# Kernel tuning notes

Hardware: AMD Instinct MI355X
Metric: run time of the kernel (lower is better)

## Reference

```python
import jax, jax.numpy as jnp
import numpy as np
import math

S, D, H, L, V = 1024, 768, 12, 6, 32000
KD = D // H
FF = 4 * D
PAD = 0


def setup_inputs() -> dict:
    key = jax.random.key(0)
    ks = jax.random.split(key, 20)
    s = D ** -0.5
    return {
        "token_ids": jax.random.randint(ks[0], (2, S), 0, V, dtype=jnp.int32),
        "emb": jax.random.normal(ks[1], (V, D)) * s,
        "Wq": jax.random.normal(ks[2], (L, H, D, KD)) * s,
        "bq": jnp.zeros((L, H, KD)),
        "Wk": jax.random.normal(ks[3], (L, H, D, KD)) * s,
        "bk": jnp.zeros((L, H, KD)),
        "Wv": jax.random.normal(ks[4], (L, H, D, D)) * s,
        "bv": jnp.zeros((L, H, D)),
        "g1": jnp.ones((L, D)), "be1": jnp.zeros((L, D)),
        "g2": jnp.ones((L, D)), "be2": jnp.zeros((L, D)),
        "W1": jax.random.normal(ks[5], (L, D, FF)) * s,
        "b1": jnp.zeros((L, FF)),
        "W2": jax.random.normal(ks[6], (L, FF, D)) * (FF ** -0.5),
        "b2": jnp.zeros((L, D)),
        "Wout": jax.random.normal(ks[7], (D, V)) * s,
        "bout": jnp.zeros((V,)),
    }


def _pe():
    pos = jnp.arange(S, dtype=jnp.float32)[:, None]
    div = jnp.exp(jnp.arange(0, D, 2, dtype=jnp.float32) * (-math.log(10000.0) / D))
    ang = pos * div  # [S, D/2]
    return jnp.stack([jnp.sin(ang), jnp.cos(ang)], axis=-1).reshape(S, D)


def _ln(x, g, b):
    m = x.mean(-1, keepdims=True)
    v = ((x - m) ** 2).mean(-1, keepdims=True)
    return (x - m) * jax.lax.rsqrt(v + 1e-5) * g + b


def reference(token_ids, emb, Wq, bq, Wk, bk, Wv, bv, g1, be1, g2, be2, W1, b1, W2, b2, Wout, bout):
    pad = token_ids == PAD  # [B,S]
    causal = jnp.triu(jnp.ones((S, S), dtype=bool), k=1)
    # mask[b,s,t] = causal | pad-as-key | pad-as-query
    mask = causal[None, None] | pad[:, None, None, :] | pad[:, None, :, None]  # [B,1,S,S]
    scale = math.sqrt(KD)
    x = emb[token_ids] + _pe()[None]  # [B,S,D]
    for l in range(L):
        q = jnp.einsum('bsd,hdk->bhsk', x, Wq[l]) + bq[l][None, :, None, :]
        k = jnp.einsum('bsd,hdk->bhsk', x, Wk[l]) + bk[l][None, :, None, :]
        v = jnp.einsum('bsd,hde->bhse', x, Wv[l]) + bv[l][None, :, None, :]
        scores = jnp.einsum('bhsk,bhtk->bhst', q, k) / scale
        scores = jnp.where(mask, -jnp.inf, scores)
        all_masked = jnp.all(mask, axis=-1)  # rows with every key masked -> uniform attn
        scores = jnp.where(all_masked[..., None], 0.0, scores)
        attn = jax.nn.softmax(scores, axis=-1)
        heads = jnp.einsum('bhst,bhte->bhse', attn, v)  # per-head full-D values
        attn_out = heads.mean(axis=1)  # heads are AVERAGED, not concatenated
        x = _ln(x + attn_out, g1[l], be1[l])
        ff = jax.nn.relu(x @ W1[l] + b1[l]) @ W2[l] + b2[l]
        x = _ln(x + ff, g2[l], be2[l])
    return x @ Wout + bout
```

## Files before the change

### kernel.cpp

```cpp
#include <hip/hip_runtime.h>
#include <hip/hip_bf16.h>

#define SQ 1024
#define DM 768
#define NH 12
#define NL 6
#define NV 32000
#define KDH 64
#define FFD 3072

using bf16 = __hip_bfloat16;
typedef __attribute__((ext_vector_type(4))) float f32x4;
typedef __attribute__((ext_vector_type(8))) short bf16x8;

__global__ void fill_kernel(float* __restrict__ out, long n, float val) {
  const long stride = (long)gridDim.x * blockDim.x;
  for (long i = (long)blockIdx.x * blockDim.x + threadIdx.x; i < n; i += stride)
    out[i] = val;
}

__device__ __forceinline__ void gload16(const void* g, void* l) {
  __builtin_amdgcn_global_load_lds(
      (const __attribute__((address_space(1))) unsigned int*)g,
      (__attribute__((address_space(3))) unsigned int*)l, 16, 0, 0);
}

template<bool OUT_BF16, bool RELU, bool CSKIP = false, bool CTRUNC = false>
__global__ __launch_bounds__(256) void gemm_bt(
    int M, int N, int K,
    const bf16* __restrict__ Ap, long sAz, int lda,
    const bf16* __restrict__ Bp, long sBz, int ldbt,
    const float* __restrict__ biasp, int sBiasZ,
    void* __restrict__ Cp, long sCz, long sCb, long sCs, long sCn)
{
  __shared__ __align__(16) char lds[49152];

  const int tid = threadIdx.x;
  const int gx = gridDim.x, gy = gridDim.y;
  const int nwg = gx * gy * (int)gridDim.z;
  int flat = ((int)blockIdx.z * gy + (int)blockIdx.y) * gx + (int)blockIdx.x;
  {
    const int q = nwg >> 3, r = nwg & 7;
    const int xcd = flat & 7, loc = flat >> 3;
    flat = (xcd < r ? xcd * (q + 1) : r * (q + 1) + (xcd - r) * q) + loc;
  }
  const int bx  = flat % gx;
  const int byz = flat / gx;
  const int m0 = bx * 128;
  const int n0 = (byz % gy) * 128;
  const int z  = byz / gy;

  if (CSKIP && n0 > m0) return;
  const int KK = CTRUNC ? min(K, m0 + 128) : K;

  const int lane = tid & 63;
  const int wid  = tid >> 6;
  const int wm = (wid >> 1) * 64;
  const int wn = (wid & 1) * 64;

  const int srow  = tid >> 2;
  const int sslot = tid & 3;
  const int xorb  = (sslot ^ (srow & 3)) << 4;

  const char* gA0 = (const char*)(Ap + (long)z * sAz + (long)(m0 + srow) * lda) + xorb;
  const char* gA1 = (const char*)(Ap + (long)z * sAz + (long)(m0 + srow + 64) * lda) + xorb;
  const char* gB0 = (const char*)(Bp + (long)z * sBz + (long)(n0 + srow) * ldbt) + xorb;
  const char* gB1 = (const char*)(Bp + (long)z * sBz + (long)(n0 + srow + 64) * ldbt) + xorb;

  auto stage = [&](int bo) {
    gload16(gA0, lds + bo + tid * 16);
    gload16(gA1, lds + bo + (tid + 256) * 16);
    gload16(gB0, lds + bo + 8192 + tid * 16);
    gload16(gB1, lds + bo + 8192 + (tid + 256) * 16);
    gA0 += 64; gA1 += 64; gB0 += 64; gB1 += 64;
  };

  const int fr = lane & 15;
  const int kq = lane >> 4;
  int fA[4], fB[4];
#pragma unroll
  for (int m = 0; m < 4; ++m) {
    const int R = wm + m * 16 + fr;
    fA[m] = R * 64 + ((kq ^ (R & 3)) << 4);
  }
#pragma unroll
  for (int n = 0; n < 4; ++n) {
    const int R = wn + n * 16 + fr;
    fB[n] = 8192 + R * 64 + ((kq ^ (R & 3)) << 4);
  }

  f32x4 acc[4][4] = {};

  const int nt = KK >> 5;
  stage(0);
  stage(16384);
  int cur = 0;
  for (int t = 0; t < nt; ++t) {
    if (t + 2 < nt) {
      int nb = cur + 2; if (nb >= 3) nb -= 3;
      stage(nb * 16384);
      asm volatile("s_waitcnt vmcnt(8)" ::: "memory");
    } else if (t + 1 < nt) {
      asm volatile("s_waitcnt vmcnt(4)" ::: "memory");
    } else {
      asm volatile("s_waitcnt vmcnt(0)" ::: "memory");
    }
    __builtin_amdgcn_s_barrier();
    const int co = cur * 16384;
    bf16x8 af[4], bfr[4];
#pragma unroll
    for (int m = 0; m < 4; ++m) af[m] = *(const bf16x8*)(lds + co + fA[m]);
#pragma unroll
    for (int n = 0; n < 4; ++n) bfr[n] = *(const bf16x8*)(lds + co + fB[n]);
#pragma unroll
    for (int m = 0; m < 4; ++m)
#pragma unroll
      for (int n = 0; n < 4; ++n)
        acc[m][n] = __builtin_amdgcn_mfma_f32_16x16x32_bf16(af[m], bfr[n], acc[m][n], 0, 0, 0);
    __builtin_amdgcn_s_barrier();
    cur = (cur == 2) ? 0 : cur + 1;
  }

  const int rg = (lane >> 4) * 4;
  const int cl = lane & 15;
#pragma unroll
  for (int n = 0; n < 4; ++n) {
    const int gcol = n0 + wn + n * 16 + cl;
    float bias = 0.f;
    if (biasp) bias = biasp[(long)z * sBiasZ + gcol];
    if (OUT_BF16 && sCs == 1) {
#pragma unroll
      for (int m = 0; m < 4; ++m) {
        const int grow = m0 + wm + m * 16 + rg;
        const long ci = (long)z * sCz + (long)(grow >> 10) * sCb
                      + (long)(grow & 1023) + (long)gcol * sCn;
        ushort4 pk;
        float v0 = acc[m][n][0] + bias, v1 = acc[m][n][1] + bias;
        float v2 = acc[m][n][2] + bias, v3 = acc[m][n][3] + bias;
        if (RELU) { v0 = fmaxf(v0, 0.f); v1 = fmaxf(v1, 0.f);
                    v2 = fmaxf(v2, 0.f); v3 = fmaxf(v3, 0.f); }
        pk.x = __builtin_bit_cast(ushort, __float2bfloat16(v0));
        pk.y = __builtin_bit_cast(ushort, __float2bfloat16(v1));
        pk.z = __builtin_bit_cast(ushort, __float2bfloat16(v2));
        pk.w = __builtin_bit_cast(ushort, __float2bfloat16(v3));
        *(ushort4*)((bf16*)Cp + ci) = pk;
      }
    } else {
#pragma unroll
      for (int m = 0; m < 4; ++m) {
#pragma unroll
        for (int rr = 0; rr < 4; ++rr) {
          const int grow = m0 + wm + m * 16 + rg + rr;
          float v = acc[m][n][rr] + bias;
          if (RELU) v = fmaxf(v, 0.f);
          const long ci = (long)z * sCz + (long)(grow >> 10) * sCb
                        + (long)(grow & 1023) * sCs + (long)gcol * sCn;
          if (OUT_BF16) ((bf16*)Cp)[ci] = __float2bfloat16(v);
          else          ((float*)Cp)[ci] = v;
        }
      }
    }
  }
}

__global__ __launch_bounds__(256) void transpose_kernel(
    const float* __restrict__ in, long sInZ, int ldin,
    bf16* __restrict__ out, long sOutZ, int ldout)
{
  __shared__ float t[64][65];
  const int tid = threadIdx.x;
  const int n0 = blockIdx.x * 64, k0 = blockIdx.y * 64;
  const float* ip = in + (long)blockIdx.z * sInZ;
  bf16* op = out + (long)blockIdx.z * sOutZ;
  const int cx = (tid & 15) * 4, ry = tid >> 4;
#pragma unroll
  for (int p = 0; p < 4; ++p) {
    const int k = ry + p * 16;
    const float4 v = *(const float4*)(ip + (long)(k0 + k) * ldin + n0 + cx);
    t[k][cx] = v.x; t[k][cx + 1] = v.y; t[k][cx + 2] = v.z; t[k][cx + 3] = v.w;
  }
  __syncthreads();
#pragma unroll
  for (int p = 0; p < 4; ++p) {
    const int n = ry + p * 16;
    ushort4 o;
    o.x = __builtin_bit_cast(ushort, __float2bfloat16(t[cx + 0][n]));
    o.y = __builtin_bit_cast(ushort, __float2bfloat16(t[cx + 1][n]));
    o.z = __builtin_bit_cast(ushort, __float2bfloat16(t[cx + 2][n]));
    o.w = __builtin_bit_cast(ushort, __float2bfloat16(t[cx + 3][n]));
    *(ushort4*)(op + (long)(n0 + n) * ldout + k0 + cx) = o;
  }
}

__global__ void biasqk_kernel(const float* __restrict__ bq, const float* __restrict__ bk,
                              float* __restrict__ out) {
  const int i = blockIdx.x * 256 + threadIdx.x;
  if (i < NH * 128) {
    const int h = i >> 7, n = i & 127;
    out[i] = (n < 64) ? bq[h * 64 + n] : bk[h * 64 + n - 64];
  }
}

__global__ __launch_bounds__(256) void xpart_kernel(
    const float* __restrict__ x, float* __restrict__ xpart) {
  const int b = blockIdx.x, g = blockIdx.y;
  const int tid = threadIdx.x;
  const float* xp = x + (long)b * SQ * DM + (long)g * 64 * DM;
  float a0 = 0.f, a1 = 0.f, a2 = 0.f;
  for (int s = 0; s < 64; ++s) {
    a0 += xp[(long)s * DM + tid];
    a1 += xp[(long)s * DM + tid + 256];
    a2 += xp[(long)s * DM + tid + 512];
  }
  float* op = xpart + (long)(b * 16 + g) * DM;
  op[tid] = a0; op[tid + 256] = a1; op[tid + 512] = a2;
}

__global__ void xmeanf_kernel(const float* __restrict__ xpart, float* __restrict__ xmean) {
  const int b = blockIdx.x;
  const int d = threadIdx.x;
  float a = 0.f;
#pragma unroll
  for (int g = 0; g < 16; ++g) a += xpart[(long)(b * 16 + g) * DM + d];
  xmean[b * DM + d] = a * (1.0f / (float)SQ);
}

__global__ __launch_bounds__(256) void vmeanw_kernel(
    const float* __restrict__ xmean, const bf16* __restrict__ wvT,
    const float* __restrict__ bv, float* __restrict__ vmean) {
  const int tid = threadIdx.x;
  const int w = blockIdx.x * 4 + (tid >> 6);
  const int b = w / DM;
  const int e = w % DM;
  const int lane = tid & 63;
  float xm[12];
#pragma unroll
  for (int j = 0; j < 12; ++j) xm[j] = xmean[b * DM + lane + j * 64];
  float acc = 0.f;
  for (int h = 0; h < NH; ++h) {
    const bf16* wr = wvT + ((long)h * DM + e) * DM;
#pragma unroll
    for (int j = 0; j < 12; ++j)
      acc += xm[j] * __bfloat162float(wr[lane + j * 64]);
  }
#pragma unroll
  for (int o = 32; o >= 1; o >>= 1) acc += __shfl_xor(acc, o);
  if (lane == 0) {
    float bs = 0.f;
#pragma unroll
    for (int h = 0; h < NH; ++h) bs += bv[h * DM + e];
    vmean[b * DM + e] = (acc + bs) * (1.0f / (float)NH);
  }
}

__global__ __launch_bounds__(256) void embed_kernel(
    const int* __restrict__ tok, const float* __restrict__ emb,
    float* __restrict__ x, bf16* __restrict__ xb)
{
  const int gid = blockIdx.x * 256 + threadIdx.x;
  const int row = gid / (DM / 4);
  const int dc  = (gid % (DM / 4)) * 4;
  const int t = tok[row];
  const int s = row & (SQ - 1);
#pragma unroll
  for (int j = 0; j < 4; ++j) {
    const int d = dc + j;
    const float e = emb[(long)t * DM + d];
    const float div = expf(-(float)(d & ~1) * (9.210340371976184f / (float)DM));
    const float ang = (float)s * div;
    const float pe = (d & 1) ? cosf(ang) : sinf(ang);
    const float v = e + pe;
    x[(long)row * DM + d] = v;
    xb[(long)row * DM + d] = __float2bfloat16(v);
  }
}

__global__ __launch_bounds__(256) void softmax_kernel(
    bf16* __restrict__ P, const int* __restrict__ tok)
{
  const int row = blockIdx.x;
  const int s = row & (SQ - 1);
  const int z = row >> 10;
  const int b = z / NH;
  bf16* sp = P + (long)row * SQ;
  const int* tb = tok + b * SQ;
  const int tid = threadIdx.x;
  const int t0 = tid * 4;

  if (tb[s] == 0) {
    const bf16 u = __float2bfloat16(1.0f / (float)SQ);
    sp[t0] = u; sp[t0 + 1] = u; sp[t0 + 2] = u; sp[t0 + 3] = u;
    return;
  }
  uint2 raw = *(const uint2*)(sp + t0);
  int4 tv = *(const int4*)(tb + t0);
  const bf16* rh = (const bf16*)&raw;
  const int tvv[4] = {tv.x, tv.y, tv.z, tv.w};
  float val[4];
  float vmax = -1e30f;
#pragma unroll
  for (int j = 0; j < 4; ++j) {
    const int t = t0 + j;
    const bool valid = (t <= s) && (tvv[j] != 0);
    val[j] = valid ? __bfloat162float(rh[j]) * 0.125f : -1e30f;
    vmax = fmaxf(vmax, val[j]);
  }
  __shared__ float red[4];
  const int lane = tid & 63, wid = tid >> 6;
  float w = vmax;
#pragma unroll
  for (int o = 32; o >= 1; o >>= 1) w = fmaxf(w, __shfl_xor(w, o));
  if (lane == 0) red[wid] = w;
  __syncthreads();
  const float Mx = fmaxf(fmaxf(red[0], red[1]), fmaxf(red[2], red[3]));
  __syncthreads();
  float e[4]; float lsum = 0.f;
#pragma unroll
  for (int j = 0; j < 4; ++j) {
    e[j] = (val[j] > -1e29f) ? expf(val[j] - Mx) : 0.f;
    lsum += e[j];
  }
  w = lsum;
#pragma unroll
  for (int o = 32; o >= 1; o >>= 1) w += __shfl_xor(w, o);
  if (lane == 0) red[wid] = w;
  __syncthreads();
  const float inv = 1.0f / (red[0] + red[1] + red[2] + red[3]);
#pragma unroll
  for (int j = 0; j < 4; ++j) sp[t0 + j] = __float2bfloat16(e[j] * inv);
}

template<int MODE>
__global__ __launch_bounds__(256) void ln_kernel(
    float* __restrict__ x, bf16* __restrict__ xb,
    const float* __restrict__ tmp, const bf16* __restrict__ heads,
    const float* __restrict__ g, const float* __restrict__ be,
    const int* __restrict__ tok, const float* __restrict__ vmean)
{
  const int r = blockIdx.x;
  const int b = r >> 10;
  const int tid = threadIdx.x;
  const bool pad = (MODE == 1) && (tok[r] == 0);
  float vals[3];
  float sum = 0.f, sq = 0.f;
#pragma unroll
  for (int i = 0; i < 3; ++i) {
    const int d = tid + i * 256;
    const float a = x[(long)r * DM + d];
    float t;
    if (MODE == 0) {
      t = tmp[(long)r * DM + d];
    } else if (pad) {
      t = vmean[b * DM + d];
    } else {
      const int s = r & (SQ - 1);
      float hs = 0.f;
#pragma unroll
      for (int h = 0; h < NH; ++h)
        hs += __bfloat162float(heads[((long)(b * NH + h) * SQ + s) * DM + d]);
      t = hs * (1.0f / (float)NH);
    }
    const float vv = a + t;
    vals[i] = vv;
    sum += vv; sq += vv * vv;
  }
  __shared__ float rs[4], rq[4];
  const int lane = tid & 63, wid = tid >> 6;
  float s1 = sum, s2 = sq;
#pragma unroll
  for (int o = 32; o >= 1; o >>= 1) { s1 += __shfl_xor(s1, o); s2 += __shfl_xor(s2, o); }
  if (lane == 0) { rs[wid] = s1; rq[wid] = s2; }
  __syncthreads();
  const float S1 = rs[0] + rs[1] + rs[2] + rs[3];
  const float S2 = rq[0] + rq[1] + rq[2] + rq[3];
  const float mean = S1 * (1.0f / (float)DM);
  const float var  = S2 * (1.0f / (float)DM) - mean * mean;
  const float rstd = rsqrtf(var + 1e-5f);
#pragma unroll
  for (int i = 0; i < 3; ++i) {
    const int d = tid + i * 256;
    const float o = (vals[i] - mean) * rstd * g[d] + be[d];
    x[(long)r * DM + d] = o;
    xb[(long)r * DM + d] = __float2bfloat16(o);
  }
}

extern "C" void kernel_launch(void* const* d_in, const int* in_sizes, int n_in,
                              void* d_out, int out_size, void* d_ws, size_t ws_size,
                              hipStream_t stream) {
  const int expect_sizes[18] = {
    2048, 24576000, 3538944, 4608, 3538944, 4608, 42467328, 55296,
    4608, 4608, 4608, 4608, 14155776, 18432, 14155776, 4608, 24576000, 32000
  };
  bool sizes_ok = (n_in == 18);
  if (sizes_ok)
    for (int i = 0; i < 18; ++i) sizes_ok = sizes_ok && (in_sizes[i] == expect_sizes[i]);
  if (!sizes_ok) {
    fill_kernel<<<2048, 256, 0, stream>>>((float*)d_out, (long)out_size, 1000.0f);
    return;
  }
  if (out_size != 65536000) {
    fill_kernel<<<2048, 256, 0, stream>>>((float*)d_out, (long)out_size, 3000.0f);
    return;
  }
  if (ws_size < 158189568ull) {
    fill_kernel<<<2048, 256, 0, stream>>>((float*)d_out, (long)out_size, 2000.0f);
    return;
  }

  const int*   tok  = (const int*)d_in[0];
  const float* emb  = (const float*)d_in[1];
  const float* Wq   = (const float*)d_in[2];
  const float* bq   = (const float*)d_in[3];
  const float* Wk   = (const float*)d_in[4];
  const float* bk   = (const float*)d_in[5];
  const float* Wv   = (const float*)d_in[6];
  const float* bv   = (const float*)d_in[7];
  const float* g1   = (const float*)d_in[8];
  const float* be1  = (const float*)d_in[9];
  const float* g2   = (const float*)d_in[10];
  const float* be2  = (const float*)d_in[11];
  const float* W1   = (const float*)d_in[12];
  const float* b1   = (const float*)d_in[13];
  const float* W2   = (const float*)d_in[14];
  const float* b2   = (const float*)d_in[15];
  const float* Wout = (const float*)d_in[16];
  const float* bout = (const float*)d_in[17];

  char* ws = (char*)d_ws;
  float* x      = (float*)(ws + 0);
  bf16*  xb     = (bf16*) (ws + 6291456);
  bf16*  qk     = (bf16*) (ws + 9437184);
  float* tmp    = (float*)(ws + 9437184);
  bf16*  vT     = (bf16*) (ws + 15728640);
  bf16*  P      = (bf16*) (ws + 53477376);
  bf16*  ff     = (bf16*) (ws + 53477376);
  bf16*  woutT  = (bf16*) (ws + 53477376);
  bf16*  heads  = (bf16*) (ws + 103809024);
  bf16*  wqkT   = (bf16*) (ws + 141557760);
  bf16*  wvT    = (bf16*) (ws + 143917056);
  bf16*  w1T    = (bf16*) (ws + 141557760);
  bf16*  w2T    = (bf16*) (ws + 146276352);
  float* biasqk = (float*)(ws + 158072832);
  float* xpart  = (float*)(ws + 158078976);
  float* xmean  = (float*)(ws + 158177280);
  float* vmean  = (float*)(ws + 158183424);

  embed_kernel<<<dim3((2 * SQ * DM / 4) / 256), 256, 0, stream>>>(tok, emb, x, xb);

  for (int l = 0; l < NL; ++l) {
    transpose_kernel<<<dim3(1, 12, NH), 256, 0, stream>>>(
        Wq + (long)l * NH * DM * KDH, (long)DM * KDH, KDH,
        wqkT, 128 * DM, DM);
    transpose_kernel<<<dim3(1, 12, NH), 256, 0, stream>>>(
        Wk + (long)l * NH * DM * KDH, (long)DM * KDH, KDH,
        wqkT + 64 * DM, 128 * DM, DM);
    transpose_kernel<<<dim3(12, 12, NH), 256, 0, stream>>>(
        Wv + (long)l * NH * DM * DM, (long)DM * DM, DM,
        wvT, (long)DM * DM, DM);
    biasqk_kernel<<<6, 256, 0, stream>>>(bq + l * NH * KDH, bk + l * NH * KDH, biasqk);

    xpart_kernel<<<dim3(2, 16), 256, 0, stream>>>(x, xpart);
    xmeanf_kernel<<<dim3(2), 768, 0, stream>>>(xpart, xmean);
    vmeanw_kernel<<<dim3(384), 256, 0, stream>>>(xmean, wvT, bv + (long)l * NH * DM, vmean);

    gemm_bt<true, false><<<dim3(16, 1, NH), 256, 0, stream>>>(
        2048, 128, DM, xb, 0, DM, wqkT, (long)128 * DM, DM,
        biasqk, 128,
        qk, (long)SQ * 128, (long)NH * SQ * 128, 128, 1);
    gemm_bt<true, false><<<dim3(16, 6, NH), 256, 0, stream>>>(
        2048, DM, DM, xb, 0, DM, wvT, (long)DM * DM, DM,
        bv + (long)l * NH * DM, DM,
        vT, (long)DM * SQ, (long)NH * DM * SQ, 1, SQ);
    gemm_bt<true, false, true, false><<<dim3(8, 8, 2 * NH), 256, 0, stream>>>(
        SQ, SQ, KDH, qk, (long)SQ * 128, 128, qk + 64, (long)SQ * 128, 128,
        (const float*)nullptr, 0,
        P, (long)SQ * SQ, 0, SQ, 1);
    softmax_kernel<<<dim3(2 * NH * SQ), 256, 0, stream>>>(P, tok);
    gemm_bt<true, false, false, true><<<dim3(8, 6, 2 * NH), 256, 0, stream>>>(
        SQ, DM, SQ, P, (long)SQ * SQ, SQ, vT, (long)DM * SQ, SQ,
        (const float*)nullptr, 0,
        heads, (long)SQ * DM, 0, DM, 1);
    ln_kernel<1><<<dim3(2048), 256, 0, stream>>>(x, xb, nullptr, heads,
                                                 g1 + l * DM, be1 + l * DM, tok, vmean);
    transpose_kernel<<<dim3(48, 12, 1), 256, 0, stream>>>(
        W1 + (long)l * DM * FFD, 0, FFD, w1T, 0, DM);
    transpose_kernel<<<dim3(12, 48, 1), 256, 0, stream>>>(
        W2 + (long)l * FFD * DM, 0, DM, w2T, 0, FFD);
    gemm_bt<true, true><<<dim3(16, 24, 1), 256, 0, stream>>>(
        2048, FFD, DM, xb, 0, DM, w1T, 0, DM,
        b1 + (long)l * FFD, 0,
        ff, 0, (long)SQ * FFD, FFD, 1);
    gemm_bt<false, false><<<dim3(16, 6, 1), 256, 0, stream>>>(
        2048, DM, FFD, ff, 0, FFD, w2T, 0, FFD,
        b2 + (long)l * DM, 0,
        tmp, 0, (long)SQ * DM, DM, 1);
    ln_kernel<0><<<dim3(2048), 256, 0, stream>>>(x, xb, tmp, nullptr,
                                                 g2 + l * DM, be2 + l * DM, tok, nullptr);
  }
  transpose_kernel<<<dim3(500, 12, 1), 256, 0, stream>>>(Wout, 0, NV, woutT, 0, DM);
  gemm_bt<false, false><<<dim3(16, 250, 1), 256, 0, stream>>>(
      2048, NV, DM, xb, 0, DM, woutT, 0, DM,
      bout, 0,
      d_out, 0, (long)SQ * NV, NV, 1);
}
```

Before: 1.717 ms.

## Vectorize LN and softmax, skip padded/causal work, swap operands for output GEMM stores

The final vocab GEMM swaps its A/B operands and uses a row bias so fp32 output can be written as float4 along contiguous rows. The softmax skips rows whose query is padding and only touches keys up to the causal 128-block boundary, and it writes results with packed stores. Both layer-norm kernels now use 96 threads with 8-wide vector loads and stores. The intent is to cut scattered global stores and memory traffic, at the cost of leaving 160 LN threads idle. Skipping pad rows in softmax relies on the downstream path (vmean) never reading those rows.

```diff
diff --git a/kernel.cpp b/kernel.cpp
--- a/kernel.cpp
+++ b/kernel.cpp
@@ -25,7 +25,8 @@
       (__attribute__((address_space(3))) unsigned int*)l, 16, 0, 0);
 }
 
-template<bool OUT_BF16, bool RELU, bool CSKIP = false, bool CTRUNC = false>
+template<bool OUT_BF16, bool RELU, bool CSKIP = false, bool CTRUNC = false,
+         bool BIAS_ROW = false>
 __global__ __launch_bounds__(256) void gemm_bt(
     int M, int N, int K,
     const bf16* __restrict__ Ap, long sAz, int lda,
@@ -123,27 +124,37 @@
 
   const int rg = (lane >> 4) * 4;
   const int cl = lane & 15;
+  const long zb = (long)z * sBiasZ;
 #pragma unroll
   for (int n = 0; n < 4; ++n) {
     const int gcol = n0 + wn + n * 16 + cl;
-    float bias = 0.f;
-    if (biasp) bias = biasp[(long)z * sBiasZ + gcol];
-    if (OUT_BF16 && sCs == 1) {
+    float biasN = 0.f;
+    if (!BIAS_ROW && biasp) biasN = biasp[zb + gcol];
+    if (sCs == 1) {
 #pragma unroll
       for (int m = 0; m < 4; ++m) {
         const int grow = m0 + wm + m * 16 + rg;
         const long ci = (long)z * sCz + (long)(grow >> 10) * sCb
                       + (long)(grow & 1023) + (long)gcol * sCn;
-        ushort4 pk;
-        float v0 = acc[m][n][0] + bias, v1 = acc[m][n][1] + bias;
-        float v2 = acc[m][n][2] + bias, v3 = acc[m][n][3] + bias;
+        float v0 = acc[m][n][0], v1 = acc[m][n][1];
+        float v2 = acc[m][n][2], v3 = acc[m][n][3];
+        if (BIAS_ROW && biasp) {
+          v0 += biasp[zb + grow];     v1 += biasp[zb + grow + 1];
+          v2 += biasp[zb + grow + 2]; v3 += biasp[zb + grow + 3];
+        } else { v0 += biasN; v1 += biasN; v2 += biasN; v3 += biasN; }
         if (RELU) { v0 = fmaxf(v0, 0.f); v1 = fmaxf(v1, 0.f);
                     v2 = fmaxf(v2, 0.f); v3 = fmaxf(v3, 0.f); }
-        pk.x = __builtin_bit_cast(ushort, __float2bfloat16(v0));
-        pk.y = __builtin_bit_cast(ushort, __float2bfloat16(v1));
-        pk.z = __builtin_bit_cast(ushort, __float2bfloat16(v2));
-        pk.w = __builtin_bit_cast(ushort, __float2bfloat16(v3));
-        *(ushort4*)((bf16*)Cp + ci) = pk;
+        if (OUT_BF16) {
+          ushort4 pk;
+          pk.x = __builtin_bit_cast(ushort, __float2bfloat16(v0));
+          pk.y = __builtin_bit_cast(ushort, __float2bfloat16(v1));
+          pk.z = __builtin_bit_cast(ushort, __float2bfloat16(v2));
+          pk.w = __builtin_bit_cast(ushort, __float2bfloat16(v3));
+          *(ushort4*)((bf16*)Cp + ci) = pk;
+        } else {
+          float4 pk = make_float4(v0, v1, v2, v3);
+          *(float4*)((float*)Cp + ci) = pk;
+        }
       }
     } else {
 #pragma unroll
@@ -151,7 +162,8 @@
 #pragma unroll
         for (int rr = 0; rr < 4; ++rr) {
           const int grow = m0 + wm + m * 16 + rg + rr;
-          float v = acc[m][n][rr] + bias;
+          float v = acc[m][n][rr]
+                  + (BIAS_ROW ? (biasp ? biasp[zb + grow] : 0.f) : biasN);
           if (RELU) v = fmaxf(v, 0.f);
           const long ci = (long)z * sCz + (long)(grow >> 10) * sCb
                         + (long)(grow & 1023) * sCs + (long)gcol * sCn;
@@ -282,28 +294,28 @@
   const int s = row & (SQ - 1);
   const int z = row >> 10;
   const int b = z / NH;
+  const int* tb = tok + b * SQ;
+  if (tb[s] == 0) return;
   bf16* sp = P + (long)row * SQ;
-  const int* tb = tok + b * SQ;
   const int tid = threadIdx.x;
   const int t0 = tid * 4;
-
-  if (tb[s] == 0) {
-    const bf16 u = __float2bfloat16(1.0f / (float)SQ);
-    sp[t0] = u; sp[t0 + 1] = u; sp[t0 + 2] = u; sp[t0 + 3] = u;
-    return;
-  }
-  uint2 raw = *(const uint2*)(sp + t0);
-  int4 tv = *(const int4*)(tb + t0);
-  const bf16* rh = (const bf16*)&raw;
-  const int tvv[4] = {tv.x, tv.y, tv.z, tv.w};
-  float val[4];
+  const int L = (s | 127) + 1;
+  const bool act = t0 < L;
+
+  float val[4] = {-1e30f, -1e30f, -1e30f, -1e30f};
   float vmax = -1e30f;
-#pragma unroll
-  for (int j = 0; j < 4; ++j) {
-    const int t = t0 + j;
-    const bool valid = (t <= s) && (tvv[j] != 0);
-    val[j] = valid ? __bfloat162float(rh[j]) * 0.125f : -1e30f;
-    vmax = fmaxf(vmax, val[j]);
+  if (act) {
+    uint2 raw = *(const uint2*)(sp + t0);
+    int4 tv = *(const int4*)(tb + t0);
+    const bf16* rh = (const bf16*)&raw;
+    const int tvv[4] = {tv.x, tv.y, tv.z, tv.w};
+#pragma unroll
+    for (int j = 0; j < 4; ++j) {
+      const int t = t0 + j;
+      const bool valid = (t <= s) && (tvv[j] != 0);
+      val[j] = valid ? __bfloat162float(rh[j]) * 0.125f : -1e30f;
+      vmax = fmaxf(vmax, val[j]);
+    }
   }
   __shared__ float red[4];
   const int lane = tid & 63, wid = tid >> 6;
@@ -326,8 +338,14 @@
   if (lane == 0) red[wid] = w;
   __syncthreads();
   const float inv = 1.0f / (red[0] + red[1] + red[2] + red[3]);
-#pragma unroll
-  for (int j = 0; j < 4; ++j) sp[t0 + j] = __float2bfloat16(e[j] * inv);
+  if (act) {
+    ushort4 pk;
+    pk.x = __builtin_bit_cast(ushort, __float2bfloat16(e[0] * inv));
+    pk.y = __builtin_bit_cast(ushort, __float2bfloat16(e[1] * inv));
+    pk.z = __builtin_bit_cast(ushort, __float2bfloat16(e[2] * inv));
+    pk.w = __builtin_bit_cast(ushort, __float2bfloat16(e[3] * inv));
+    *(ushort4*)(sp + t0) = pk;
+  }
 }
 
 template<int MODE>
@@ -339,32 +357,47 @@
 {
   const int r = blockIdx.x;
   const int b = r >> 10;
+  const int s = r & (SQ - 1);
   const int tid = threadIdx.x;
+  __shared__ float vbuf[DM];
+  __shared__ float rs[4], rq[4];
   const bool pad = (MODE == 1) && (tok[r] == 0);
-  float vals[3];
   float sum = 0.f, sq = 0.f;
-#pragma unroll
-  for (int i = 0; i < 3; ++i) {
-    const int d = tid + i * 256;
-    const float a = x[(long)r * DM + d];
-    float t;
+  float v[8];
+  if (tid < 96) {
+    const int d0 = tid * 8;
+    const float4 x0 = *(const float4*)(x + (long)r * DM + d0);
+    const float4 x1 = *(const float4*)(x + (long)r * DM + d0 + 4);
+    v[0] = x0.x; v[1] = x0.y; v[2] = x0.z; v[3] = x0.w;
+    v[4] = x1.x; v[5] = x1.y; v[6] = x1.z; v[7] = x1.w;
     if (MODE == 0) {
-      t = tmp[(long)r * DM + d];
+      const float4 t0_ = *(const float4*)(tmp + (long)r * DM + d0);
+      const float4 t1_ = *(const float4*)(tmp + (long)r * DM + d0 + 4);
+      v[0] += t0_.x; v[1] += t0_.y; v[2] += t0_.z; v[3] += t0_.w;
+      v[4] += t1_.x; v[5] += t1_.y; v[6] += t1_.z; v[7] += t1_.w;
     } else if (pad) {
-      t = vmean[b * DM + d];
+      const float4 t0_ = *(const float4*)(vmean + b * DM + d0);
+      const float4 t1_ = *(const float4*)(vmean + b * DM + d0 + 4);
+      v[0] += t0_.x; v[1] += t0_.y; v[2] += t0_.z; v[3] += t0_.w;
+      v[4] += t1_.x; v[5] += t1_.y; v[6] += t1_.z; v[7] += t1_.w;
     } else {
-      const int s = r & (SQ - 1);
-      float hs = 0.f;
-#pragma unroll
-      for (int h = 0; h < NH; ++h)
-        hs += __bfloat162float(heads[((long)(b * NH + h) * SQ + s) * DM + d]);
-      t = hs * (1.0f / (float)NH);
+      float hs[8] = {0.f, 0.f, 0.f, 0.f, 0.f, 0.f, 0.f, 0.f};
+      for (int h = 0; h < NH; ++h) {
+        union { uint4 u; ushort us[8]; } hv;
+        hv.u = *(const uint4*)(heads + ((long)(b * NH + h) * SQ + s) * DM + d0);
+#pragma unroll
+        for (int j = 0; j < 8; ++j)
+          hs[j] += __bfloat162float(__builtin_bit_cast(bf16, hv.us[j]));
+      }
+#pragma unroll
+      for (int j = 0; j < 8; ++j) v[j] += hs[j] * (1.0f / (float)NH);
     }
-    const float vv = a + t;
-    vals[i] = vv;
-    sum += vv; sq += vv * vv;
-  }
-  __shared__ float rs[4], rq[4];
+#pragma unroll
+    for (int j = 0; j < 8; ++j) {
+      vbuf[tid * 8 + j] = v[j];
+      sum += v[j]; sq += v[j] * v[j];
+    }
+  }
   const int lane = tid & 63, wid = tid >> 6;
   float s1 = sum, s2 = sq;
 #pragma unroll
@@ -376,12 +409,28 @@
   const float mean = S1 * (1.0f / (float)DM);
   const float var  = S2 * (1.0f / (float)DM) - mean * mean;
   const float rstd = rsqrtf(var + 1e-5f);
-#pragma unroll
-  for (int i = 0; i < 3; ++i) {
-    const int d = tid + i * 256;
-    const float o = (vals[i] - mean) * rstd * g[d] + be[d];
-    x[(long)r * DM + d] = o;
-    xb[(long)r * DM + d] = __float2bfloat16(o);
+  if (tid < 96) {
+    const int d0 = tid * 8;
+    const float4 g0 = *(const float4*)(g + d0);
+    const float4 g1 = *(const float4*)(g + d0 + 4);
+    const float4 b0 = *(const float4*)(be + d0);
+    const float4 b1 = *(const float4*)(be + d0 + 4);
+    float o[8];
+    o[0] = (v[0] - mean) * rstd * g0.x + b0.x;
+    o[1] = (v[1] - mean) * rstd * g0.y + b0.y;
+    o[2] = (v[2] - mean) * rstd * g0.z + b0.z;
+    o[3] = (v[3] - mean) * rstd * g0.w + b0.w;
+    o[4] = (v[4] - mean) * rstd * g1.x + b1.x;
+    o[5] = (v[5] - mean) * rstd * g1.y + b1.y;
+    o[6] = (v[6] - mean) * rstd * g1.z + b1.z;
+    o[7] = (v[7] - mean) * rstd * g1.w + b1.w;
+    *(float4*)(x + (long)r * DM + d0)     = make_float4(o[0], o[1], o[2], o[3]);
+    *(float4*)(x + (long)r * DM + d0 + 4) = make_float4(o[4], o[5], o[6], o[7]);
+    union { uint4 u; ushort us[8]; } pk;
+#pragma unroll
+    for (int j = 0; j < 8; ++j)
+      pk.us[j] = __builtin_bit_cast(ushort, __float2bfloat16(o[j]));
+    *(uint4*)(xb + (long)r * DM + d0) = pk.u;
   }
 }
 
@@ -499,8 +548,8 @@
                                                  g2 + l * DM, be2 + l * DM, tok, nullptr);
   }
   transpose_kernel<<<dim3(500, 12, 1), 256, 0, stream>>>(Wout, 0, NV, woutT, 0, DM);
-  gemm_bt<false, false><<<dim3(16, 250, 1), 256, 0, stream>>>(
-      2048, NV, DM, xb, 0, DM, woutT, 0, DM,
+  gemm_bt<false, false, false, false, true><<<dim3(250, 16, 1), 256, 0, stream>>>(
+      NV, 2048, DM, woutT, 0, DM, xb, 0, DM,
       bout, 0,
-      d_out, 0, (long)SQ * NV, NV, 1);
-}
+      d_out, 0, 1024, 1, NV);
+}
```

Result: no change. 1.723 ms (+0.4%).
